# Kernel tuning notes

Hardware: AMD Instinct MI355X
Metric: run time of the kernel (lower is better)

## Reference

```python
import jax, jax.numpy as jnp
import numpy as np

B, M, D = 512, 96, 512
H = 8            # num_heads
DH = D // H      # head dim
NC = 3           # num_clusters
BETA = 5
MEM = 1024       # memory_size
EPS = 1e-8


def _l2norm(x, axis=-1):
    # torch F.cosine_similarity clamps each norm at eps=1e-8
    n = jnp.linalg.norm(x, axis=axis, keepdims=True)
    return x / jnp.maximum(n, EPS)


def _dynamic_clustering(sims):
    # sims: (B, M). Sort descending, split into NC equal groups,
    # per-group mean and (unbiased) std. (dynamic_clustering is not
    # defined in the source repo; this is the assumed implementation.)
    s = -jnp.sort(-sims, axis=1)               # descending
    g = s.reshape(B, NC, M // NC)
    means = g.mean(axis=-1)                    # (B, NC)
    stds = jnp.std(g, axis=-1, ddof=1)         # (B, NC)
    return means, stds


def setup_inputs() -> dict:
    key = jax.random.key(0)
    ks = jax.random.split(key, 6)
    vis_global = jax.random.normal(ks[0], (B, D), dtype=jnp.float32)
    text_features = jax.random.normal(ks[1], (B, M, D), dtype=jnp.float32)
    scale = 1.0 / np.sqrt(D)
    in_proj_w = jax.random.normal(ks[2], (3 * D, D), dtype=jnp.float32) * scale
    in_proj_b = jnp.zeros((3 * D,), dtype=jnp.float32)
    out_proj_w = jax.random.normal(ks[3], (D, D), dtype=jnp.float32) * scale
    out_proj_b = jnp.zeros((D,), dtype=jnp.float32)
    text_memory = jax.random.normal(ks[4], (MEM, D), dtype=jnp.float32)
    tau_p_log = jnp.log(jnp.asarray(0.1, dtype=jnp.float32))
    tau_n_log = jnp.log(jnp.asarray(0.05, dtype=jnp.float32))
    return dict(vis_global=vis_global, text_features=text_features,
                in_proj_w=in_proj_w, in_proj_b=in_proj_b,
                out_proj_w=out_proj_w, out_proj_b=out_proj_b,
                text_memory=text_memory, tau_p_log=tau_p_log, tau_n_log=tau_n_log)


def reference(vis_global, text_features, in_proj_w, in_proj_b,
              out_proj_w, out_proj_b, text_memory, tau_p_log, tau_n_log):
    # --- dynamic clustering over visual-text cosine sims ---
    sims = jnp.einsum('bd,bmd->bm', _l2norm(vis_global), _l2norm(text_features))
    means, stds = _dynamic_clustering(sims)
    cluster_scores = means / (stds + 1e-6)     # (B, NC)

    # --- MultiheadAttention: 1-token query, M-token key/value ---
    wq, wk, wv = in_proj_w[:D], in_proj_w[D:2 * D], in_proj_w[2 * D:]
    bq, bk, bv = in_proj_b[:D], in_proj_b[D:2 * D], in_proj_b[2 * D:]
    q = (vis_global @ wq.T + bq).reshape(B, H, DH)              # (B,H,DH)
    k = (text_features @ wk.T + bk).reshape(B, M, H, DH)        # (B,M,H,DH)
    v = (text_features @ wv.T + bv).reshape(B, M, H, DH)
    attn = jax.nn.softmax(jnp.einsum('bhd,bmhd->bhm', q, k) / np.sqrt(DH), axis=-1)
    ctx = jnp.einsum('bhm,bmhd->bhd', attn, v).reshape(B, D)
    corrected = ctx @ out_proj_w.T + out_proj_b                 # (B, D)

    tau_p = jnp.exp(tau_p_log)
    tau_n = jnp.exp(tau_n_log)
    pos_sim = jnp.sum(_l2norm(vis_global) * _l2norm(corrected), axis=-1)  # (B,)

    # memory-bank scatter (ptr starts at 0) + negatives, all detached
    corr_sg = jax.lax.stop_gradient(corrected)
    mem = text_memory.at[0:B].set(corr_sg)
    all_negs = jnp.concatenate([jnp.roll(corr_sg, 1, axis=0), mem], axis=0)  # (B+MEM, D)

    neg_sims = _l2norm(vis_global) @ _l2norm(all_negs).T        # (B, B+MEM)
    hard_negs, _ = jax.lax.top_k(neg_sims, BETA)                # (B, BETA)

    pos_term = jnp.exp(pos_sim / tau_p)
    neg_terms = jnp.exp(hard_negs / tau_n).sum(axis=1)
    loss = -jnp.mean(jnp.log(pos_term / (pos_term + neg_terms + 1e-8)))
    return loss, corrected, cluster_scores
```

## Files before the change

### kernel.cpp

```cpp
#include <hip/hip_runtime.h>
#include <math.h>

typedef unsigned short u16;
typedef unsigned int u32;
typedef __attribute__((ext_vector_type(8))) short short8;
typedef __attribute__((ext_vector_type(4))) float f32x4;

#define EPS 1e-8f

__device__ inline float bf2f(u16 u) {
    union { u32 i; float f; } v; v.i = ((u32)u) << 16; return v.f;
}
__device__ inline u16 f2bf(float f) {
    union { float f; u32 u; } v; v.f = f;
    u32 r = v.u + 0x7fffu + ((v.u >> 16) & 1u);
    return (u16)(r >> 16);
}
__device__ inline u32 pack2(float a, float b) {
    return (u32)f2bf(a) | ((u32)f2bf(b) << 16);
}
__device__ inline float wave_sum(float v) {
    for (int off = 32; off; off >>= 1) v += __shfl_xor(v, off, 64);
    return v;
}

__global__ __launch_bounds__(256) void prep_vis(const float* __restrict__ vis,
                                                float* __restrict__ vis_n,
                                                u16* __restrict__ vis_nb,
                                                u16* __restrict__ vis_b,
                                                float* __restrict__ loss0)
{
    if (blockIdx.x == 0 && threadIdx.x == 0) loss0[0] = 0.0f;
    int wave = threadIdx.x >> 6, lane = threadIdx.x & 63;
    int b = blockIdx.x * 4 + wave;
    const float* row = vis + b * 512 + lane * 8;
    float4 x0 = *(const float4*)row;
    float4 x1 = *(const float4*)(row + 4);
    uint4 rk;
    rk.x = pack2(x0.x, x0.y); rk.y = pack2(x0.z, x0.w);
    rk.z = pack2(x1.x, x1.y); rk.w = pack2(x1.z, x1.w);
    *(uint4*)(vis_b + b*512 + lane*8) = rk;
    float ss = x0.x*x0.x + x0.y*x0.y + x0.z*x0.z + x0.w*x0.w
             + x1.x*x1.x + x1.y*x1.y + x1.z*x1.z + x1.w*x1.w;
    ss = wave_sum(ss);
    float inv = 1.0f / fmaxf(sqrtf(ss), EPS);
    float4 y0, y1;
    y0.x = x0.x*inv; y0.y = x0.y*inv; y0.z = x0.z*inv; y0.w = x0.w*inv;
    y1.x = x1.x*inv; y1.y = x1.y*inv; y1.z = x1.z*inv; y1.w = x1.w*inv;
    *(float4*)(vis_n + b*512 + lane*8)     = y0;
    *(float4*)(vis_n + b*512 + lane*8 + 4) = y1;
    uint4 pk;
    pk.x = pack2(y0.x, y0.y); pk.y = pack2(y0.z, y0.w);
    pk.z = pack2(y1.x, y1.y); pk.w = pack2(y1.z, y1.w);
    *(uint4*)(vis_nb + b*512 + lane*8) = pk;
}

__global__ __launch_bounds__(256) void cvt3(const float* __restrict__ ipw,
                                            const float* __restrict__ opw,
                                            u16* __restrict__ wqb,
                                            u16* __restrict__ wvb,
                                            u16* __restrict__ wob)
{
    int i = (blockIdx.x * 256 + threadIdx.x) * 4;
    const float* src; u16* dst; int j;
    if (i < 262144)      { j = i;          src = ipw + j;          dst = wqb + j; }
    else if (i < 524288) { j = i - 262144; src = ipw + 524288 + j; dst = wvb + j; }
    else                 { j = i - 524288; src = opw + j;          dst = wob + j; }
    float4 v = *(const float4*)src;
    uint2 pk; pk.x = pack2(v.x, v.y); pk.y = pack2(v.z, v.w);
    *(uint2*)dst = pk;
}

__global__ __launch_bounds__(256) void gemm64(const u16* __restrict__ A, int lda,
                                              const u16* __restrict__ B,
                                              const float* __restrict__ bias,
                                              float* __restrict__ Cf, int ldc)
{
    __shared__ __align__(16) u16 As[64 * 64];
    __shared__ __align__(16) u16 Bs[64 * 64];
    const int t = threadIdx.x, lane = t & 63, w = t >> 6;
    const int m0 = blockIdx.x * 64, n0 = blockIdx.y * 64;
    const int wm = (w >> 1) * 32, wn = (w & 1) * 32;
    const int l16 = lane & 15, quad = lane >> 4;
    const int srow = t >> 3, scol = (t & 7) * 8;

    f32x4 acc[2][2];
    for (int i = 0; i < 2; i++)
        for (int j = 0; j < 2; j++)
            for (int e = 0; e < 4; e++) acc[i][j][e] = 0.f;

    for (int ko = 0; ko < 512; ko += 64) {
        __syncthreads();
        #pragma unroll
        for (int i = 0; i < 2; i++) {
            int row = i * 32 + srow;
            *(uint4*)&As[row * 64 + scol] = *(const uint4*)&A[(size_t)(m0 + row) * lda + ko + scol];
            *(uint4*)&Bs[row * 64 + scol] = *(const uint4*)&B[(size_t)(n0 + row) * 512 + ko + scol];
        }
        __syncthreads();
        #pragma unroll
        for (int ks = 0; ks < 2; ks++) {
            short8 af[2], bfr[2];
            #pragma unroll
            for (int i = 0; i < 2; i++)
                af[i] = *(const short8*)&As[(wm + i * 16 + l16) * 64 + ks * 32 + quad * 8];
            #pragma unroll
            for (int j = 0; j < 2; j++)
                bfr[j] = *(const short8*)&Bs[(wn + j * 16 + l16) * 64 + ks * 32 + quad * 8];
            #pragma unroll
            for (int i = 0; i < 2; i++)
                #pragma unroll
                for (int j = 0; j < 2; j++)
                    acc[i][j] = __builtin_amdgcn_mfma_f32_16x16x32_bf16(af[i], bfr[j], acc[i][j], 0, 0, 0);
        }
    }
    for (int i = 0; i < 2; i++) {
        int row = m0 + wm + i * 16 + quad * 4;
        for (int j = 0; j < 2; j++) {
            int col = n0 + wn + j * 16 + l16;
            float bv = bias ? bias[col] : 0.f;
            for (int r = 0; r < 4; r++)
                Cf[(size_t)(row + r) * ldc + col] = acc[i][j][r] + bv;
        }
    }
}

__global__ __launch_bounds__(256) void gemm_head(const u16* __restrict__ u_allb,
                                                 const u16* __restrict__ wvb,
                                                 const float* __restrict__ bv,
                                                 u16* __restrict__ ctxb)
{
    const int h = blockIdx.y;
    const u16* A = u_allb + h * 512;
    const u16* B = wvb + (size_t)h * 64 * 512;
    __shared__ __align__(16) u16 As[64 * 64];
    __shared__ __align__(16) u16 Bs[64 * 64];
    const int t = threadIdx.x, lane = t & 63, w = t >> 6;
    const int m0 = blockIdx.x * 64;
    const int wm = (w >> 1) * 32, wn = (w & 1) * 32;
    const int l16 = lane & 15, quad = lane >> 4;
    const int srow = t >> 3, scol = (t & 7) * 8;

    f32x4 acc[2][2];
    for (int i = 0; i < 2; i++)
        for (int j = 0; j < 2; j++)
            for (int e = 0; e < 4; e++) acc[i][j][e] = 0.f;

    for (int ko = 0; ko < 512; ko += 64) {
        __syncthreads();
        #pragma unroll
        for (int i = 0; i < 2; i++) {
            int row = i * 32 + srow;
            *(uint4*)&As[row * 64 + scol] = *(const uint4*)&A[(size_t)(m0 + row) * 4096 + ko + scol];
            *(uint4*)&Bs[row * 64 + scol] = *(const uint4*)&B[(size_t)row * 512 + ko + scol];
        }
        __syncthreads();
        #pragma unroll
        for (int ks = 0; ks < 2; ks++) {
            short8 af[2], bfr[2];
            #pragma unroll
            for (int i = 0; i < 2; i++)
                af[i] = *(const short8*)&As[(wm + i * 16 + l16) * 64 + ks * 32 + quad * 8];
            #pragma unroll
            for (int j = 0; j < 2; j++)
                bfr[j] = *(const short8*)&Bs[(wn + j * 16 + l16) * 64 + ks * 32 + quad * 8];
            #pragma unroll
            for (int i = 0; i < 2; i++)
                #pragma unroll
                for (int j = 0; j < 2; j++)
                    acc[i][j] = __builtin_amdgcn_mfma_f32_16x16x32_bf16(af[i], bfr[j], acc[i][j], 0, 0, 0);
        }
    }
    for (int i = 0; i < 2; i++) {
        int row = m0 + wm + i * 16 + quad * 4;
        for (int j = 0; j < 2; j++) {
            int col = wn + j * 16 + l16;
            float bb = bv[h * 64 + col];
            for (int r = 0; r < 4; r++)
                ctxb[(size_t)(row + r) * 512 + h * 64 + col] = f2bf(acc[i][j][r] + bb);
        }
    }
}

__global__ __launch_bounds__(256) void qk_proj(const float* __restrict__ q,
                                               const float* __restrict__ wk,
                                               float* __restrict__ qk_all)
{
    int bg = blockIdx.x, h = blockIdx.y;
    int t = threadIdx.x;
    int j = blockIdx.z * 256 + t;
    __shared__ float q8[8][64];
    {
        int r = t >> 5;
        int d0 = (t & 31) * 2;
        const float* qp = q + (bg * 8 + r) * 512 + h * 64 + d0;
        q8[r][d0] = qp[0]; q8[r][d0 + 1] = qp[1];
    }
    __syncthreads();
    float acc[8] = {0, 0, 0, 0, 0, 0, 0, 0};
    const float* wrow = wk + (size_t)(h * 64) * 512 + j;
    #pragma unroll 4
    for (int d = 0; d < 64; d++) {
        float ww = wrow[(size_t)d * 512];
        #pragma unroll
        for (int r = 0; r < 8; r++) acc[r] += q8[r][d] * ww;
    }
    #pragma unroll
    for (int r = 0; r < 8; r++)
        qk_all[((size_t)(bg * 8 + r) * 8 + h) * 512 + j] = acc[r];
}

__global__ __launch_bounds__(512) void fused_attn(const float* __restrict__ tf,
                                                  const float* __restrict__ vis_n,
                                                  const float* __restrict__ qk_all,
                                                  u16* __restrict__ u_allb,
                                                  float* __restrict__ out_cs)
{
    __shared__ __align__(16) u16 Xs[96 * 520];
    __shared__ __align__(16) u16 Qs[16 * 520];
    __shared__ __align__(16) u16 Ps[16 * 104];
    __shared__ float Sc[16 * 100];
    __shared__ float sm_[96], srt[96], linv[8];

    const int b = blockIdx.x;
    const int t = threadIdx.x, w = t >> 6, lane = t & 63;
    const int l16 = lane & 15, quad = lane >> 4;

    const float4* v4 = (const float4*)(vis_n + b * 512 + lane * 8);
    float4 va = v4[0], vb = v4[1];

    {
        const float4* q4 = (const float4*)(qk_all + ((size_t)b * 8 + w) * 512 + lane * 8);
        float4 a = q4[0], c = q4[1];
        uint4 pk;
        pk.x = pack2(a.x, a.y); pk.y = pack2(a.z, a.w);
        pk.z = pack2(c.x, c.y); pk.w = pack2(c.z, c.w);
        *(uint4*)&Qs[w * 520 + lane * 8] = pk;
    }

    #pragma unroll 2
    for (int i = 0; i < 12; i++) {
        int m = w + i * 8;
        const float4* x4 = (const float4*)(tf + ((size_t)b * 96 + m) * 512 + lane * 8);
        float4 a = x4[0], c = x4[1];
        float ss = a.x*a.x + a.y*a.y + a.z*a.z + a.w*a.w
                 + c.x*c.x + c.y*c.y + c.z*c.z + c.w*c.w;
        float dt = a.x*va.x + a.y*va.y + a.z*va.z + a.w*va.w
                 + c.x*vb.x + c.y*vb.y + c.z*vb.z + c.w*vb.w;
        ss = wave_sum(ss);
        dt = wave_sum(dt);
        if (lane == 0) sm_[m] = dt / fmaxf(sqrtf(ss), EPS);
        uint4 pk;
        pk.x = pack2(a.x, a.y); pk.y = pack2(a.z, a.w);
        pk.z = pack2(c.x, c.y); pk.w = pack2(c.z, c.w);
        *(uint4*)&Xs[m * 520 + lane * 8] = pk;
    }
    __syncthreads();

    if (w < 6) {
        f32x4 acc;
        for (int e = 0; e < 4; e++) acc[e] = 0.f;
        #pragma unroll
        for (int ks = 0; ks < 16; ks++) {
            short8 a = *(const short8*)&Xs[(w * 16 + l16) * 520 + ks * 32 + quad * 8];
            short8 q = *(const short8*)&Qs[l16 * 520 + ks * 32 + quad * 8];
            acc = __builtin_amdgcn_mfma_f32_16x16x32_bf16(a, q, acc, 0, 0, 0);
        }
        #pragma unroll
        for (int r = 0; r < 4; r++)
            Sc[l16 * 100 + w * 16 + quad * 4 + r] = acc[r] * 0.125f;
    }
    __syncthreads();

    {
        float e0 = __expf(Sc[w * 100 + lane]);
        float e1 = (lane < 32) ? __expf(Sc[w * 100 + 64 + lane]) : 0.f;
        float l = wave_sum(e0 + e1);
        Ps[w * 104 + lane] = f2bf(e0);
        if (lane < 32) Ps[w * 104 + 64 + lane] = f2bf(e1);
        if (lane == 0) linv[w] = 1.0f / l;
    }
    if (t < 96) {
        float v = sm_[t]; int r = 0;
        for (int j = 0; j < 96; j++) {
            float u = sm_[j];
            r += (u > v) || (u == v && j < t);
        }
        srt[r] = v;
    }
    __syncthreads();

    #pragma unroll
    for (int jj = 0; jj < 4; jj++) {
        int n0 = (w * 4 + jj) * 16;
        f32x4 acc;
        for (int e = 0; e < 4; e++) acc[e] = 0.f;
        #pragma unroll
        for (int ks = 0; ks < 3; ks++) {
            short8 ap = *(const short8*)&Ps[l16 * 104 + ks * 32 + quad * 8];
            short8 bx;
            #pragma unroll
            for (int j = 0; j < 8; j++)
                bx[j] = (short)Xs[(ks * 32 + quad * 8 + j) * 520 + n0 + l16];
            acc = __builtin_amdgcn_mfma_f32_16x16x32_bf16(ap, bx, acc, 0, 0, 0);
        }
        if (quad < 2) {
            #pragma unroll
            for (int r = 0; r < 4; r++) {
                int h = quad * 4 + r;
                u_allb[((size_t)b * 8 + h) * 512 + n0 + l16] = f2bf(acc[r] * linv[h]);
            }
        }
    }
    if (t < 3) {
        float mean = 0.f;
        #pragma unroll 8
        for (int i = 0; i < 32; i++) mean += srt[t * 32 + i];
        mean *= (1.0f / 32.0f);
        float var = 0.f;
        #pragma unroll 8
        for (int i = 0; i < 32; i++) { float d = srt[t * 32 + i] - mean; var += d * d; }
        var *= (1.0f / 31.0f);
        out_cs[b * 3 + t] = mean / (sqrtf(var) + 1e-6f);
    }
}

__global__ __launch_bounds__(256) void negs_build(const float* __restrict__ corrected,
                                                  const float* __restrict__ tm,
                                                  const float* __restrict__ vis_n,
                                                  u16* __restrict__ negs_nb,
                                                  float* __restrict__ pos)
{
    int wave = threadIdx.x >> 6, lane = threadIdx.x & 63;
    int j = blockIdx.x * 4 + wave;
    const float* src = (j < 512) ? (corrected + j * 512) : (tm + j * 512);
    const float* row = src + lane * 8;
    float4 x0 = *(const float4*)row;
    float4 x1 = *(const float4*)(row + 4);
    float ss = x0.x*x0.x + x0.y*x0.y + x0.z*x0.z + x0.w*x0.w
             + x1.x*x1.x + x1.y*x1.y + x1.z*x1.z + x1.w*x1.w;
    float dt = 0.f;
    if (j < 512) {
        const float* vn = vis_n + j * 512 + lane * 8;
        float4 v0 = *(const float4*)vn;
        float4 v1 = *(const float4*)(vn + 4);
        dt = x0.x*v0.x + x0.y*v0.y + x0.z*v0.z + x0.w*v0.w
           + x1.x*v1.x + x1.y*v1.y + x1.z*v1.z + x1.w*v1.w;
    }
    ss = wave_sum(ss);
    dt = wave_sum(dt);
    float inv = 1.0f / fmaxf(sqrtf(ss), EPS);
    float4 y0, y1;
    y0.x = x0.x*inv; y0.y = x0.y*inv; y0.z = x0.z*inv; y0.w = x0.w*inv;
    y1.x = x1.x*inv; y1.y = x1.y*inv; y1.z = x1.z*inv; y1.w = x1.w*inv;
    uint4 pk;
    pk.x = pack2(y0.x, y0.y); pk.y = pack2(y0.z, y0.w);
    pk.z = pack2(y1.x, y1.y); pk.w = pack2(y1.z, y1.w);
    *(uint4*)(negs_nb + j * 512 + lane * 8) = pk;
    if (j < 512 && lane == 0) pos[j] = dt * inv;
}

__global__ __launch_bounds__(256) void topk_loss(const float* __restrict__ ns,
                                                 const float* __restrict__ pos,
                                                 const float* __restrict__ tau_p_log,
                                                 const float* __restrict__ tau_n_log,
                                                 float* __restrict__ out_loss)
{
    int b = blockIdx.x, t = threadIdx.x;
    __shared__ float sv[1536];
    __shared__ float rv[256];
    __shared__ int   ri[256];
    __shared__ float stop5[5];
    const float* row = ns + b * 1024;
    for (int i = t; i < 1536; i += 256) {
        float v;
        if (i < 1024) v = row[i & 511];
        else          v = row[512 + (i - 1024)];
        sv[i] = v;
    }
    __syncthreads();
    for (int r = 0; r < 5; r++) {
        float best = -1e30f; int bi = 0;
        for (int i = t; i < 1536; i += 256)
            if (sv[i] > best) { best = sv[i]; bi = i; }
        rv[t] = best; ri[t] = bi;
        __syncthreads();
        for (int s = 128; s > 0; s >>= 1) {
            if (t < s) {
                if (rv[t + s] > rv[t]) { rv[t] = rv[t + s]; ri[t] = ri[t + s]; }
            }
            __syncthreads();
        }
        if (t == 0) { stop5[r] = rv[0]; sv[ri[0]] = -1e30f; }
        __syncthreads();
    }
    if (t == 0) {
        float tp = expf(tau_p_log[0]), tn = expf(tau_n_log[0]);
        float p = expf(pos[b] / tp);
        float n = 0.f;
        for (int r = 0; r < 5; r++) n += expf(stop5[r] / tn);
        float term = logf(p / (p + n + 1e-8f));
        atomicAdd(out_loss, -term * (1.0f / 512.0f));
    }
}

extern "C" void kernel_launch(void* const* d_in, const int* in_sizes, int n_in,
                              void* d_out, int out_size, void* d_ws, size_t ws_size,
                              hipStream_t stream) {
    const float* vis = (const float*)d_in[0];
    const float* tf  = (const float*)d_in[1];
    const float* ipw = (const float*)d_in[2];
    const float* ipb = (const float*)d_in[3];
    const float* opw = (const float*)d_in[4];
    const float* opb = (const float*)d_in[5];
    const float* tm  = (const float*)d_in[6];
    const float* tpl = (const float*)d_in[7];
    const float* tnl = (const float*)d_in[8];

    float* out       = (float*)d_out;
    float* out_loss  = out;
    float* out_corr  = out + 1;
    float* out_cs    = out + 1 + 512 * 512;

    char* p = (char*)d_ws;
    auto alloc = [&](size_t bytes) { char* r = p; p += (bytes + 255) & ~(size_t)255; return r; };
    float* vis_n  = (float*)alloc(512 * 512 * 4);
    u16*   vis_nb = (u16*)  alloc(512 * 512 * 2);
    u16*   vis_b  = (u16*)  alloc(512 * 512 * 2);
    u16*   wqb    = (u16*)  alloc(512 * 512 * 2);
    u16*   wvb    = (u16*)  alloc(512 * 512 * 2);
    u16*   wob    = (u16*)  alloc(512 * 512 * 2);
    float* qws    = (float*)alloc(512 * 512 * 4);
    float* qk_all = (float*)alloc((size_t)512 * 8 * 512 * 4);
    u16*   u_allb = (u16*)  alloc((size_t)512 * 8 * 512 * 2);
    u16*   ctxb   = (u16*)  alloc(512 * 512 * 2);
    u16*   negsb  = (u16*)  alloc(1024 * 512 * 2);
    float* ns     = (float*)alloc(512 * 1024 * 4);
    float* pos    = (float*)alloc(512 * 4);

    const float* wk = ipw + 512 * 512;
    const float* bv = ipb + 2 * 512;

    prep_vis<<<128, 256, 0, stream>>>(vis, vis_n, vis_nb, vis_b, out_loss);
    cvt3<<<768, 256, 0, stream>>>(ipw, opw, wqb, wvb, wob);
    gemm64<<<dim3(8, 8), 256, 0, stream>>>(vis_b, 512, wqb, ipb, qws, 512);
    qk_proj<<<dim3(64, 8, 2), 256, 0, stream>>>(qws, wk, qk_all);
    fused_attn<<<512, 512, 0, stream>>>(tf, vis_n, qk_all, u_allb, out_cs);
    gemm_head<<<dim3(8, 8), 256, 0, stream>>>(u_allb, wvb, bv, ctxb);
    gemm64<<<dim3(8, 8), 256, 0, stream>>>(ctxb, 512, wob, opb, out_corr, 512);
    negs_build<<<256, 256, 0, stream>>>(out_corr, tm, vis_n, negsb, pos);
    gemm64<<<dim3(8, 16), 256, 0, stream>>>(vis_nb, 512, negsb, nullptr, ns, 1024);
    topk_loss<<<512, 256, 0, stream>>>(ns, pos, tpl, tnl, out_loss);
}
```

Measured before the change: 253.4 us.

## Merge prep kernels, pair row loads in attention, rewrite top-k as wave merge

Merges the visual-normalization and weight-conversion kernels into one launch to remove a launch. In fused_attn, each wave now processes two text rows per iteration so their loads and shuffle reductions interleave and raise memory-level parallelism. The top-k loss kernel is replaced: each thread sorts its four values locally, and five rounds of wave-shuffle argmax plus a cross-wave pick merge them. The first 512 entries are counted twice, because they appear both as rolled negatives and in the memory bank. This removes the shared-memory tree reduction and its many barriers, but the duplicate counting relies on the rolled set being a permutation of the written memory rows.

```diff
diff --git a/kernel.cpp b/kernel.cpp
--- a/kernel.cpp
+++ b/kernel.cpp
@@ -24,15 +24,32 @@
     return v;
 }
 
-__global__ __launch_bounds__(256) void prep_vis(const float* __restrict__ vis,
-                                                float* __restrict__ vis_n,
-                                                u16* __restrict__ vis_nb,
-                                                u16* __restrict__ vis_b,
-                                                float* __restrict__ loss0)
-{
-    if (blockIdx.x == 0 && threadIdx.x == 0) loss0[0] = 0.0f;
+__global__ __launch_bounds__(256) void prep(const float* __restrict__ vis,
+                                            const float* __restrict__ ipw,
+                                            const float* __restrict__ opw,
+                                            float* __restrict__ vis_n,
+                                            u16* __restrict__ vis_nb,
+                                            u16* __restrict__ vis_b,
+                                            u16* __restrict__ wqb,
+                                            u16* __restrict__ wvb,
+                                            u16* __restrict__ wob,
+                                            float* __restrict__ loss0)
+{
+    int bid = blockIdx.x;
+    if (bid >= 128) {
+        int i = ((bid - 128) * 256 + threadIdx.x) * 4;
+        const float* src; u16* dst; int j;
+        if (i < 262144)      { j = i;          src = ipw + j;          dst = wqb + j; }
+        else if (i < 524288) { j = i - 262144; src = ipw + 524288 + j; dst = wvb + j; }
+        else                 { j = i - 524288; src = opw + j;          dst = wob + j; }
+        float4 v = *(const float4*)src;
+        uint2 pk; pk.x = pack2(v.x, v.y); pk.y = pack2(v.z, v.w);
+        *(uint2*)dst = pk;
+        return;
+    }
+    if (bid == 0 && threadIdx.x == 0) loss0[0] = 0.0f;
     int wave = threadIdx.x >> 6, lane = threadIdx.x & 63;
-    int b = blockIdx.x * 4 + wave;
+    int b = bid * 4 + wave;
     const float* row = vis + b * 512 + lane * 8;
     float4 x0 = *(const float4*)row;
     float4 x1 = *(const float4*)(row + 4);
@@ -55,22 +72,6 @@
     *(uint4*)(vis_nb + b*512 + lane*8) = pk;
 }
 
-__global__ __launch_bounds__(256) void cvt3(const float* __restrict__ ipw,
-                                            const float* __restrict__ opw,
-                                            u16* __restrict__ wqb,
-                                            u16* __restrict__ wvb,
-                                            u16* __restrict__ wob)
-{
-    int i = (blockIdx.x * 256 + threadIdx.x) * 4;
-    const float* src; u16* dst; int j;
-    if (i < 262144)      { j = i;          src = ipw + j;          dst = wqb + j; }
-    else if (i < 524288) { j = i - 262144; src = ipw + 524288 + j; dst = wvb + j; }
-    else                 { j = i - 524288; src = opw + j;          dst = wob + j; }
-    float4 v = *(const float4*)src;
-    uint2 pk; pk.x = pack2(v.x, v.y); pk.y = pack2(v.z, v.w);
-    *(uint2*)dst = pk;
-}
-
 __global__ __launch_bounds__(256) void gemm64(const u16* __restrict__ A, int lda,
                                               const u16* __restrict__ B,
                                               const float* __restrict__ bias,
@@ -239,21 +240,39 @@
     }
 
     #pragma unroll 2
-    for (int i = 0; i < 12; i++) {
-        int m = w + i * 8;
-        const float4* x4 = (const float4*)(tf + ((size_t)b * 96 + m) * 512 + lane * 8);
-        float4 a = x4[0], c = x4[1];
-        float ss = a.x*a.x + a.y*a.y + a.z*a.z + a.w*a.w
-                 + c.x*c.x + c.y*c.y + c.z*c.z + c.w*c.w;
-        float dt = a.x*va.x + a.y*va.y + a.z*va.z + a.w*va.w
-                 + c.x*vb.x + c.y*vb.y + c.z*vb.z + c.w*vb.w;
-        ss = wave_sum(ss);
-        dt = wave_sum(dt);
-        if (lane == 0) sm_[m] = dt / fmaxf(sqrtf(ss), EPS);
-        uint4 pk;
-        pk.x = pack2(a.x, a.y); pk.y = pack2(a.z, a.w);
-        pk.z = pack2(c.x, c.y); pk.w = pack2(c.z, c.w);
-        *(uint4*)&Xs[m * 520 + lane * 8] = pk;
+    for (int i = 0; i < 6; i++) {
+        int m0r = w + i * 16;
+        int m1r = m0r + 8;
+        const float4* x4a = (const float4*)(tf + ((size_t)b * 96 + m0r) * 512 + lane * 8);
+        const float4* x4b = (const float4*)(tf + ((size_t)b * 96 + m1r) * 512 + lane * 8);
+        float4 a0 = x4a[0], c0 = x4a[1];
+        float4 a1 = x4b[0], c1 = x4b[1];
+        float ss0 = a0.x*a0.x + a0.y*a0.y + a0.z*a0.z + a0.w*a0.w
+                  + c0.x*c0.x + c0.y*c0.y + c0.z*c0.z + c0.w*c0.w;
+        float dt0 = a0.x*va.x + a0.y*va.y + a0.z*va.z + a0.w*va.w
+                  + c0.x*vb.x + c0.y*vb.y + c0.z*vb.z + c0.w*vb.w;
+        float ss1 = a1.x*a1.x + a1.y*a1.y + a1.z*a1.z + a1.w*a1.w
+                  + c1.x*c1.x + c1.y*c1.y + c1.z*c1.z + c1.w*c1.w;
+        float dt1 = a1.x*va.x + a1.y*va.y + a1.z*va.z + a1.w*va.w
+                  + c1.x*vb.x + c1.y*vb.y + c1.z*vb.z + c1.w*vb.w;
+        #pragma unroll
+        for (int off = 32; off; off >>= 1) {
+            ss0 += __shfl_xor(ss0, off, 64);
+            dt0 += __shfl_xor(dt0, off, 64);
+            ss1 += __shfl_xor(ss1, off, 64);
+            dt1 += __shfl_xor(dt1, off, 64);
+        }
+        if (lane == 0) {
+            sm_[m0r] = dt0 / fmaxf(sqrtf(ss0), EPS);
+            sm_[m1r] = dt1 / fmaxf(sqrtf(ss1), EPS);
+        }
+        uint4 pk0, pk1;
+        pk0.x = pack2(a0.x, a0.y); pk0.y = pack2(a0.z, a0.w);
+        pk0.z = pack2(c0.x, c0.y); pk0.w = pack2(c0.z, c0.w);
+        pk1.x = pack2(a1.x, a1.y); pk1.y = pack2(a1.z, a1.w);
+        pk1.z = pack2(c1.x, c1.y); pk1.w = pack2(c1.z, c1.w);
+        *(uint4*)&Xs[m0r * 520 + lane * 8] = pk0;
+        *(uint4*)&Xs[m1r * 520 + lane * 8] = pk1;
     }
     __syncthreads();
 
@@ -367,39 +386,59 @@
                                                  float* __restrict__ out_loss)
 {
     int b = blockIdx.x, t = threadIdx.x;
-    __shared__ float sv[1536];
-    __shared__ float rv[256];
-    __shared__ int   ri[256];
-    __shared__ float stop5[5];
-    const float* row = ns + b * 1024;
-    for (int i = t; i < 1536; i += 256) {
-        float v;
-        if (i < 1024) v = row[i & 511];
-        else          v = row[512 + (i - 1024)];
-        sv[i] = v;
-    }
-    __syncthreads();
-    for (int r = 0; r < 5; r++) {
-        float best = -1e30f; int bi = 0;
-        for (int i = t; i < 1536; i += 256)
-            if (sv[i] > best) { best = sv[i]; bi = i; }
-        rv[t] = best; ri[t] = bi;
-        __syncthreads();
-        for (int s = 128; s > 0; s >>= 1) {
-            if (t < s) {
-                if (rv[t + s] > rv[t]) { rv[t] = rv[t + s]; ri[t] = ri[t + s]; }
-            }
-            __syncthreads();
-        }
-        if (t == 0) { stop5[r] = rv[0]; sv[ri[0]] = -1e30f; }
-        __syncthreads();
-    }
+    int w = t >> 6, lane = t & 63;
+    __shared__ float cand_v[4];
+    __shared__ int   cand_m[4];
+
+    const float4 raw = *(const float4*)(ns + b * 1024 + t * 4);
+    float lv[4] = {raw.x, raw.y, raw.z, raw.w};
+    #pragma unroll
+    for (int i = 1; i < 4; i++) {
+        float key = lv[i];
+        int j = i - 1;
+        #pragma unroll
+        for (int k = 0; k < 3; k++) {
+            if (j >= 0 && lv[j] < key) { lv[j + 1] = lv[j]; j--; }
+        }
+        lv[j + 1] = key;
+    }
+    const int mult = (t < 128) ? 2 : 1;
+    int lp = 0;
+
+    float tn = expf(tau_n_log[0]);
+    float inv_tn = 1.0f / tn;
+    float nsum = 0.f;
+    int collected = 0;
+
+    for (int round = 0; round < 5 && collected < 5; round++) {
+        float head = (lp < 4) ? lv[lp] : -1e30f;
+        float mv = head; int ml = lane;
+        #pragma unroll
+        for (int off = 32; off; off >>= 1) {
+            float ov = __shfl_xor(mv, off, 64);
+            int   ol = __shfl_xor(ml, off, 64);
+            if (ov > mv || (ov == mv && ol < ml)) { mv = ov; ml = ol; }
+        }
+        if (lane == 0) { cand_v[w] = mv; cand_m[w] = ml; }
+        __syncthreads();
+        float bv = cand_v[0]; int bw = 0;
+        #pragma unroll
+        for (int i = 1; i < 4; i++) {
+            if (cand_v[i] > bv) { bv = cand_v[i]; bw = i; }
+        }
+        int bl = cand_m[bw];
+        __syncthreads();
+        if (w == bw && lane == bl) lp++;
+        int wm = ((bw * 64 + bl) < 128) ? 2 : 1;
+        int take = (wm < (5 - collected)) ? wm : (5 - collected);
+        nsum += (float)take * __expf(bv * inv_tn);
+        collected += take;
+    }
+
     if (t == 0) {
-        float tp = expf(tau_p_log[0]), tn = expf(tau_n_log[0]);
+        float tp = expf(tau_p_log[0]);
         float p = expf(pos[b] / tp);
-        float n = 0.f;
-        for (int r = 0; r < 5; r++) n += expf(stop5[r] / tn);
-        float term = logf(p / (p + n + 1e-8f));
+        float term = logf(p / (p + nsum + 1e-8f));
         atomicAdd(out_loss, -term * (1.0f / 512.0f));
     }
 }
@@ -441,8 +480,7 @@
     const float* wk = ipw + 512 * 512;
     const float* bv = ipb + 2 * 512;
 
-    prep_vis<<<128, 256, 0, stream>>>(vis, vis_n, vis_nb, vis_b, out_loss);
-    cvt3<<<768, 256, 0, stream>>>(ipw, opw, wqb, wvb, wob);
+    prep<<<896, 256, 0, stream>>>(vis, ipw, opw, vis_n, vis_nb, vis_b, wqb, wvb, wob, out_loss);
     gemm64<<<dim3(8, 8), 256, 0, stream>>>(vis_b, 512, wqb, ipb, qws, 512);
     qk_proj<<<dim3(64, 8, 2), 256, 0, stream>>>(qws, wk, qk_all);
     fused_attn<<<512, 512, 0, stream>>>(tf, vis_n, qk_all, u_allb, out_cs);
```

Measured after the change: 250.5 us. No clear change (-1.1%).
